# Optimization experiments

Measured on AMD Instinct MI355X. Metric: run time of the kernel, lower is better.

Reference implementation:

```python
import jax, jax.numpy as jnp
import numpy as np

L, B, D, H = 128, 4, 768, 300
NT, NR = 7, 12  # ner tags, relation types
EPS = 1e-5


def _cummax(v):
    # torch: cumsum(softmax(v, -1), -1)
    return jnp.cumsum(jax.nn.softmax(v, axis=-1), axis=-1)


def _layernorm(v, g, b):
    mu = jnp.mean(v, axis=-1, keepdims=True)
    var = jnp.var(v, axis=-1, keepdims=True)
    return (v - mu) * jax.lax.rsqrt(var + EPS) * g + b


def setup_inputs() -> dict:
    key = jax.random.key(0)
    ks = jax.random.split(key, 24)
    s = lambda fan_in: 1.0 / np.sqrt(fan_in)
    u = lambda k, shape, sc: jax.random.uniform(k, shape, jnp.float32, -sc, sc)
    inp = {
        "x": jax.random.normal(ks[0], (L, B, D), jnp.float32),
        "mask": jnp.ones((L, B), jnp.float32),
        # PFN_Unit
        "W_ih": u(ks[1], (5 * H, D), s(D)), "b_ih": u(ks[2], (5 * H,), s(D)),
        "W_hh": u(ks[3], (5 * H, H), s(H)), "b_hh": u(ks[4], (5 * H,), s(H)),
        "W_tr": u(ks[5], (H, 3 * H), s(3 * H)), "b_tr": u(ks[6], (H,), s(3 * H)),
        # NERUnit
        "n_W": u(ks[7], (H, 2 * H), s(2 * H)), "n_b": u(ks[8], (H,), s(2 * H)),
        "ner_hW": u(ks[9], (H, 3 * H), s(3 * H)), "ner_hb": u(ks[10], (H,), s(3 * H)),
        "ner_g": jnp.ones((H,), jnp.float32), "ner_beta": jnp.zeros((H,), jnp.float32),
        "ner_tW": u(ks[11], (NT, H), s(H)), "ner_tb": u(ks[12], (NT,), s(H)),
        # ReUnit
        "r_W": u(ks[13], (H, 2 * H), s(2 * H)), "r_b": u(ks[14], (H,), s(2 * H)),
        "re_hW": u(ks[15], (H, 3 * H), s(3 * H)), "re_hb": u(ks[16], (H,), s(3 * H)),
        "re_g": jnp.ones((H,), jnp.float32), "re_beta": jnp.zeros((H,), jnp.float32),
        "re_tW": u(ks[17], (NR, H), s(H)), "re_tb": u(ks[18], (NR,), s(H)),
    }
    return inp


def _encoder(x, W_ih, b_ih, W_hh, b_hh, W_tr, b_tr):
    pre = jnp.einsum('lbd,gd->lbg', x, W_ih) + b_ih  # precompute input transform [L,B,5H]

    def step(carry, gx):
        h, c_in = carry
        gates = gx + h @ W_hh.T + b_hh
        c, eg_cin, rg_cin, eg_c, rg_c = jnp.split(gates, 5, axis=1)
        eg_cin, rg_cin = 1.0 - _cummax(eg_cin), _cummax(rg_cin)
        eg_c, rg_c = 1.0 - _cummax(eg_c), _cummax(rg_c)
        c = jnp.tanh(c)
        ov_c = rg_c * eg_c
        up_c, dn_c = rg_c - ov_c, eg_c - ov_c
        ov_i = rg_cin * eg_cin
        up_i, dn_i = rg_cin - ov_i, eg_cin - ov_i
        share = ov_i * c_in + ov_c * c
        c_re = up_i * c_in + up_c * c + share
        c_ner = dn_i * c_in + dn_c * c + share
        c_out = jnp.concatenate([c_re, c_ner, share], axis=-1) @ W_tr.T + b_tr
        h_out = jnp.tanh(c_out)
        return (h_out, c_out), (jnp.tanh(c_ner), jnp.tanh(c_re), jnp.tanh(share))

    h0 = jnp.zeros((x.shape[1], W_hh.shape[1]), x.dtype)
    _, (h_ner, h_re, h_share) = jax.lax.scan(step, (h0, h0), pre)
    return h_ner, h_re, h_share  # each [L,B,H]


def _pair_unit(h_task, h_share, mask, gW, gb, hW, hb, ln_g, ln_b, tW, tb, diag):
    length = h_task.shape[0]
    # global feature: tanh(Linear(cat(share, task))), max over time
    h_glob = jnp.tanh(jnp.concatenate([h_share, h_task], axis=-1) @ gW.T + gb)  # [L,B,H]
    g = jnp.max(h_glob, axis=0)  # [B,H]
    # pairwise feature [L,L,B,3H] = cat(start, end, global)
    st = jnp.broadcast_to(h_task[:, None], (length, length) + h_task.shape[1:])
    en = jnp.broadcast_to(h_task[None, :], (length, length) + h_task.shape[1:])
    gb4 = jnp.broadcast_to(g, (length, length) + g.shape)
    feat = jnp.concatenate([st, en, gb4], axis=-1)
    out = _layernorm(feat @ hW.T + hb, ln_g, ln_b)
    out = jax.nn.elu(out)  # eval mode: dropout is identity
    out = jax.nn.sigmoid(out @ tW.T + tb)  # [L,L,B,T]
    # mask
    m = mask[:, None, :] * mask[None, :, :]  # [L,L,B]
    if diag:
        m = m * jnp.triu(jnp.ones((length, length), out.dtype))[:, :, None]
    return out * m[..., None]


def reference(x, mask, W_ih, b_ih, W_hh, b_hh, W_tr, b_tr,
              n_W, n_b, ner_hW, ner_hb, ner_g, ner_beta, ner_tW, ner_tb,
              r_W, r_b, re_hW, re_hb, re_g, re_beta, re_tW, re_tb):
    h_ner, h_re, h_share = _encoder(x, W_ih, b_ih, W_hh, b_hh, W_tr, b_tr)
    ner = _pair_unit(h_ner, h_share, mask, n_W, n_b, ner_hW, ner_hb,
                     ner_g, ner_beta, ner_tW, ner_tb, diag=True)
    re = _pair_unit(h_re, h_share, mask, r_W, r_b, re_hW, re_hb,
                    re_g, re_beta, re_tW, re_tb, diag=False)
    return ner, re
```

## Files before the change

kernel.cpp:

```cpp
#include <hip/hip_runtime.h>

#define LLEN 128
#define BB 4
#define DD 768
#define HH 300
#define G5 1500
#define H3 900
#define NTT 7
#define NRR 12
#define NCHB 10
#define RPB 150
#define OPB 30

#define C_WIH  0
#define C_X    1152000
#define C_WHH2 1545216
#define C_WTR2 1995216
#define F_BIH  2265216
#define F_BTR  2266720
#define F_PRE  2267040
#define F_HG0  (F_PRE)
#define F_HG1  (F_PRE+153600)
#define F_A0   (F_PRE+307200)
#define F_E0   (F_PRE+460800)
#define F_GF0  (F_PRE+616832)
#define F_GF1  (F_PRE+618048)
#define F_HNER (F_PRE+768000)
#define F_HRE  (F_HNER+153600)
#define F_HSH  (F_HRE+153600)
#define F_A1   0
#define F_E1   153600
#define F_AUX  (F_HSH+153600)
#define P_CPUB 192000
#define AUXB   2432
#define AUX_FL 9728
#define WS_NEED_BYTES ((size_t)(F_AUX+11776)*4)

typedef unsigned short u16;
typedef unsigned int u32;
typedef float f4 __attribute__((ext_vector_type(4)));
typedef int i4 __attribute__((ext_vector_type(4)));

__device__ __forceinline__ float bf2f(u16 u) {
  union { u32 i; float f; } v; v.i = ((u32)u) << 16; return v.f;
}
__device__ __forceinline__ u16 f2bf(float f) {
  union { float f; u32 i; } v; v.f = f;
  u32 r = v.i + 0x7fffu + ((v.i >> 16) & 1u);
  return (u16)(r >> 16);
}
__device__ __forceinline__ float ldin(const void* p, int i, bool f32) {
  return f32 ? ((const float*)p)[i] : bf2f(((const u16*)p)[i]);
}
__device__ __forceinline__ bool is32(const void* mk) {
  return ((const u16*)mk)[0] == 0;
}
__device__ __forceinline__ float wsum(float x) {
  #pragma unroll
  for (int d = 1; d < 64; d <<= 1) x += __shfl_xor(x, d);
  return x;
}
__device__ __forceinline__ void astore(float* p, float v) {
  union { float f; int i; } u; u.f = v;
  __hip_atomic_store((int*)p, u.i, __ATOMIC_RELAXED, __HIP_MEMORY_SCOPE_AGENT);
}
__device__ __forceinline__ void gbar(int* flag, int tid, int target) {
  __syncthreads();
  if (tid == 0) {
    __builtin_amdgcn_s_waitcnt(0);
    __hip_atomic_fetch_add(flag, 1, __ATOMIC_RELAXED, __HIP_MEMORY_SCOPE_AGENT);
    int it = 0;
    while (__hip_atomic_load(flag, __ATOMIC_RELAXED, __HIP_MEMORY_SCOPE_AGENT) < target) {
      __builtin_amdgcn_s_sleep(1);
      if (++it > 50000) break;
    }
  }
  __syncthreads();
}
__device__ __forceinline__ f4 ld4x(const f4* p, int mode) {
  f4 v;
  if (mode)
    asm volatile("global_load_dwordx4 %0, %1, off sc0\n\ts_waitcnt vmcnt(0)"
                 : "=v"(v) : "v"(p) : "memory");
  else
    asm volatile("global_load_dwordx4 %0, %1, off sc0 sc1\n\ts_waitcnt vmcnt(0)"
                 : "=v"(v) : "v"(p) : "memory");
  return v;
}
__device__ __forceinline__ float ld1x(const float* p, int mode) {
  float v;
  if (mode)
    asm volatile("global_load_dword %0, %1, off sc0\n\ts_waitcnt vmcnt(0)"
                 : "=v"(v) : "v"(p) : "memory");
  else
    asm volatile("global_load_dword %0, %1, off sc0 sc1\n\ts_waitcnt vmcnt(0)"
                 : "=v"(v) : "v"(p) : "memory");
  return v;
}
__device__ __forceinline__ int ldix(const int* p, int mode) {
  int v;
  if (mode)
    asm volatile("global_load_dword %0, %1, off sc0\n\ts_waitcnt vmcnt(0)"
                 : "=v"(v) : "v"(p) : "memory");
  else
    asm volatile("global_load_dword %0, %1, off sc0 sc1\n\ts_waitcnt vmcnt(0)"
                 : "=v"(v) : "v"(p) : "memory");
  return v;
}
__device__ __forceinline__ void exst(float* p, float v, int mode) {
  if (mode) *p = v; else astore(p, v);
}
__device__ __forceinline__ void ld9(const float* base,
                                    f4& a0, f4& a1, f4& a2, f4& a3, f4& a4,
                                    f4& a5, f4& a6, f4& a7, f4& a8) {
  asm volatile(
    "global_load_dwordx4 %0, %9, off sc0\n\t"
    "global_load_dwordx4 %1, %9, off offset:16 sc0\n\t"
    "global_load_dwordx4 %2, %9, off offset:32 sc0\n\t"
    "global_load_dwordx4 %3, %9, off offset:64 sc0\n\t"
    "global_load_dwordx4 %4, %9, off offset:80 sc0\n\t"
    "global_load_dwordx4 %5, %9, off offset:96 sc0\n\t"
    "global_load_dwordx4 %6, %9, off offset:128 sc0\n\t"
    "global_load_dwordx4 %7, %9, off offset:144 sc0\n\t"
    "global_load_dwordx4 %8, %9, off offset:160 sc0\n\t"
    "s_waitcnt vmcnt(0)"
    : "=&v"(a0), "=&v"(a1), "=&v"(a2), "=&v"(a3), "=&v"(a4),
      "=&v"(a5), "=&v"(a6), "=&v"(a7), "=&v"(a8)
    : "v"(base) : "memory");
}
__device__ __forceinline__ int poll10(const int* slots, int tok, int mode) {
  i4 a, b, c;
  if (mode)
    asm volatile("global_load_dwordx4 %0, %3, off sc0\n\t"
                 "global_load_dwordx4 %1, %4, off sc0\n\t"
                 "global_load_dwordx4 %2, %5, off sc0\n\t"
                 "s_waitcnt vmcnt(0)"
                 : "=&v"(a), "=&v"(b), "=&v"(c)
                 : "v"(slots), "v"(slots + 4), "v"(slots + 8) : "memory");
  else
    asm volatile("global_load_dwordx4 %0, %3, off sc0 sc1\n\t"
                 "global_load_dwordx4 %1, %4, off sc0 sc1\n\t"
                 "global_load_dwordx4 %2, %5, off sc0 sc1\n\t"
                 "s_waitcnt vmcnt(0)"
                 : "=&v"(a), "=&v"(b), "=&v"(c)
                 : "v"(slots), "v"(slots + 4), "v"(slots + 8) : "memory");
  return (a.x >= tok) & (a.y >= tok) & (a.z >= tok) & (a.w >= tok) &
         (b.x >= tok) & (b.y >= tok) & (b.z >= tok) & (b.w >= tok) &
         (c.x >= tok) & (c.y >= tok);
}
__device__ __forceinline__ void sbar(int* slots, int ch, int tok, int tid, int mode) {
  asm volatile("s_waitcnt vmcnt(0)" ::: "memory");
  __syncthreads();
  if (tid == 0) {
    if (mode) slots[ch] = tok;
    else __hip_atomic_store(slots + ch, tok, __ATOMIC_RELAXED, __HIP_MEMORY_SCOPE_AGENT);
  }
  if (tid < 64) {
    int it = 0;
    while (!poll10(slots, tok, mode)) {
      __builtin_amdgcn_s_sleep(1);
      if (++it > 5000) break;
    }
  }
  __syncthreads();
}
__device__ __forceinline__ void sbarA(int* slots, int* abf, int ch, int tok, int tid,
                                      volatile int* s_fail) {
  asm volatile("s_waitcnt vmcnt(0)" ::: "memory");
  __syncthreads();
  if (tid == 0)
    __hip_atomic_store(slots + ch, tok, __ATOMIC_RELAXED, __HIP_MEMORY_SCOPE_AGENT);
  if (tid < 64) {
    int it = 0;
    while (!poll10(slots, tok, 0)) {
      __builtin_amdgcn_s_sleep(1);
      ++it;
      if ((it & 255) == 0 &&
          __hip_atomic_load(abf, __ATOMIC_RELAXED, __HIP_MEMORY_SCOPE_AGENT) != 0) {
        *s_fail = 1; break;
      }
      if (it > 8000) {
        __hip_atomic_store(abf, 1, __ATOMIC_RELAXED, __HIP_MEMORY_SCOPE_AGENT);
        *s_fail = 1; break;
      }
    }
  }
  __syncthreads();
}
__device__ __forceinline__ int claim_bc(int* cl, int nb) {
  unsigned xcd;
  asm volatile("s_getreg_b32 %0, hwreg(HW_REG_XCC_ID)" : "=s"(xcd));
  xcd &= 7u;
  int rank = __hip_atomic_fetch_add(cl + xcd, 1, __ATOMIC_RELAXED, __HIP_MEMORY_SCOPE_AGENT);
  __hip_atomic_fetch_add(cl + 8, 1, __ATOMIC_RELAXED, __HIP_MEMORY_SCOPE_AGENT);
  int it = 0;
  while (__hip_atomic_load(cl + 8, __ATOMIC_RELAXED, __HIP_MEMORY_SCOPE_AGENT) < nb) {
    __builtin_amdgcn_s_sleep(2);
    if (++it > 100000) break;
  }
  int base = 0;
  for (unsigned x = 0; x < xcd; ++x)
    base += __hip_atomic_load(cl + x, __ATOMIC_RELAXED, __HIP_MEMORY_SCOPE_AGENT) / NCHB;
  int cnt = __hip_atomic_load(cl + xcd, __ATOMIC_RELAXED, __HIP_MEMORY_SCOPE_AGENT);
  int slot = base + rank / NCHB;
  return (rank < (cnt / NCHB) * NCHB && slot < BB) ? (slot * 16 + rank % NCHB) : -1;
}

__global__ void k_canon(const void* xo, const void* mk, const void* Wih, const void* bih,
                        const void* Whh, const void* bhh, const void* Wtr, const void* btr,
                        float* ws) {
  bool f32 = is32(mk);
  int piece = blockIdx.y;
  int i = blockIdx.x * 256 + threadIdx.x;
  switch (piece) {
    case 0: if (!f32 && i < 1152000) ws[C_WIH + i] = ldin(Wih, i, f32); break;
    case 1: if (!f32 && i < 393216)  ws[C_X + i]   = ldin(xo, i, f32);  break;
    case 2: if (i < 225000) {
      int k2 = i / G5, out = i - k2 * G5;
      float2 v;
      v.x = ldin(Whh, out * HH + 2 * k2, f32);
      v.y = ldin(Whh, out * HH + 2 * k2 + 1, f32);
      ((float2*)(ws + C_WHH2))[i] = v;
    } break;
    case 3: if (i < 135000) {
      int k2 = i / HH, out = i - k2 * HH;
      float2 v;
      v.x = ldin(Wtr, out * H3 + 2 * k2, f32);
      v.y = ldin(Wtr, out * H3 + 2 * k2 + 1, f32);
      ((float2*)(ws + C_WTR2))[i] = v;
    } break;
    case 4: {
      if (i < 1504) ws[F_BIH + i] = (i < G5) ? ldin(bih, i, f32) + ldin(bhh, i, f32) : 0.f;
      else if (i < 1824) { int j = i - 1504; ws[F_BTR + j] = (j < HH) ? ldin(btr, j, f32) : 0.f; }
    } break;
    case 5: {
      if (i < AUX_FL) ws[F_AUX + i] = 0.f;
      else if (i < 11776) {
        int* ip = (int*)(ws + F_AUX + AUX_FL);
        __hip_atomic_store(ip + (i - AUX_FL), 0, __ATOMIC_RELAXED, __HIP_MEMORY_SCOPE_AGENT);
      }
    } break;
  }
}

__global__ void k_pre2(const void* xo, const void* Wo, const void* mk,
                       const float* cX, const float* cW, const float* biasf, float* pre) {
  bool f32 = is32(mk);
  const float* X = f32 ? (const float*)xo : cX;
  const float* W = f32 ? (const float*)Wo : cW;
  __shared__ __align__(16) float xl[8 * DD];
  int tid = threadIdx.x;
  int lb0 = (blockIdx.x >> 1) * 8;
  int half = blockIdx.x & 1;
  for (int e = tid; e < 8 * DD; e += 256) xl[e] = X[(size_t)lb0 * DD + e];
  __syncthreads();
  for (int j = half * 750 + tid; j < half * 750 + 750; j += 256) {
    const float4* w = (const float4*)(W + (size_t)j * DD);
    float acc[8] = {0.f, 0.f, 0.f, 0.f, 0.f, 0.f, 0.f, 0.f};
    #pragma unroll 2
    for (int k = 0; k < DD / 4; ++k) {
      float4 u = w[k];
      #pragma unroll
      for (int r = 0; r < 8; ++r) {
        const float4 p = *(const float4*)(xl + r * DD + k * 4);
        acc[r] += u.x * p.x + u.y * p.y + u.z * p.z + u.w * p.w;
      }
    }
    float bias = biasf[j];
    #pragma unroll
    for (int r = 0; r < 8; ++r) pre[(size_t)(lb0 + r) * G5 + j] = acc[r] + bias;
  }
}

__global__ void __launch_bounds__(512, 2) k_scanA(const float* pre, const float2* W2h, const float2* W2t,
                                                  const float* btrf, float* hner, float* hre, float* hsh,
                                                  float* aux, float* xw) {
  __shared__ __align__(16) float ga_l[1504];
  __shared__ __align__(16) float vv_l[1204];
  __shared__ __align__(16) float tnh_l[304];
  __shared__ __align__(16) float cat_l[904];
  __shared__ __align__(16) float ci_l[304];
  __shared__ __align__(16) float ps[512];
  __shared__ __align__(16) float h_loc[32];
  __shared__ int s_bc;
  __shared__ int s_fail;
  int tid = threadIdx.x;
  int* ibase = (int*)(aux + AUX_FL);
  if (tid == 0) { s_bc = claim_bc(ibase, (int)gridDim.x); s_fail = 0; }
  __syncthreads();
  int bc = s_bc;
  if (bc < 0) return;
  int b = bc >> 4, ch = bc & 15;
  int* slots = ibase + 32 + b * 64;
  int* abf   = slots + 24;
  int* done  = ibase + 1536;

  if (ch < 2) {
    float* pb0 = xw + (size_t)ch * 96000 + b * 24000;
    for (int i = tid; i < 3000; i += 512) {
      int row = i >> 1, col = 10 + (i & 1);
      pb0[row * 16 + col] = 0.f;
    }
  }

  int o0 = 3 * tid;
  float2 wh2[45];
  if (tid < 500) {
    #pragma unroll
    for (int j = 0; j < 3; ++j)
      #pragma unroll
      for (int kk = 0; kk < 15; ++kk)
        wh2[j * 15 + kk] = W2h[(size_t)(ch * 15 + kk) * G5 + (o0 + j)];
  }
  int o2 = tid % OPB, jj = tid / OPB;
  float2 wt[29];
  int k2b = jj * 29;
  int k2e = (k2b + 29 < 450) ? (k2b + 29) : 450;
  int nk2 = k2e - k2b;
  if (tid < 480) {
    const float2* wp = W2t + (size_t)k2b * HH + (ch * OPB + o2);
    #pragma unroll
    for (int q = 0; q < 29; ++q) if (q < nk2) wt[q] = wp[(size_t)q * HH];
  }
  float pv0 = 0.f, pv1 = 0.f, pv2 = 0.f;
  if (tid < 500) {
    const float* pr = pre + (size_t)b * G5 + o0;
    pv0 = pr[0]; pv1 = pr[1]; pv2 = pr[2];
  }
  __syncthreads();

  for (int t = 0; t < LLEN; ++t) {
    int buf = t & 1;
    float* pb = xw + (size_t)buf * 96000 + b * 24000;
    if (t > 0) {
      if (tid < 500) {
        float2 h2[15];
        #pragma unroll
        for (int kk = 0; kk < 15; ++kk) h2[kk] = *(const float2*)(h_loc + 2 * kk);
        #pragma unroll
        for (int j = 0; j < 3; ++j) {
          float acc = 0.f;
          #pragma unroll
          for (int kk = 0; kk < 15; ++kk)
            acc += wh2[j * 15 + kk].x * h2[kk].x + wh2[j * 15 + kk].y * h2[kk].y;
          pb[(size_t)(o0 + j) * 16 + ch] = acc;
        }
      }
      sbarA(slots, abf, ch, t, tid, &s_fail);
      if (s_fail) return;
      if (tid < 500) {
        f4 a0, a1, a2, a3, a4, a5, a6, a7, a8;
        ld9(pb + (size_t)o0 * 16, a0, a1, a2, a3, a4, a5, a6, a7, a8);
        ga_l[o0]     = pv0 + (((a0.x + a0.y) + (a0.z + a0.w)) +
                              ((a1.x + a1.y) + (a1.z + a1.w)) +
                              ((a2.x + a2.y) + (a2.z + a2.w)));
        ga_l[o0 + 1] = pv1 + (((a3.x + a3.y) + (a3.z + a3.w)) +
                              ((a4.x + a4.y) + (a4.z + a4.w)) +
                              ((a5.x + a5.y) + (a5.z + a5.w)));
        ga_l[o0 + 2] = pv2 + (((a6.x + a6.y) + (a6.z + a6.w)) +
                              ((a7.x + a7.y) + (a7.z + a7.w)) +
                              ((a8.x + a8.y) + (a8.z + a8.w)));
      }
      if (tid < 75) {
        const float* cp = xw + P_CPUB + (size_t)(((t - 1) & 1) * 4 + b) * 304;
        f4 v = ld4x((const f4*)cp + tid, 1);
        *(f4*)(ci_l + 4 * tid) = v;
      }
    } else {
      if (tid < 500) { ga_l[o0] = pv0; ga_l[o0 + 1] = pv1; ga_l[o0 + 2] = pv2; }
    }
    __syncthreads();
    if (tid < HH) tnh_l[tid] = tanhf(ga_l[tid]);
    {
      int w = tid >> 6, ln = tid & 63;
      if (w >= 4) {
        int c = w - 3;
        const float* g = ga_l + c * 300;
        int e0 = ln * 5;
        float ex0 = 0.f, ex1 = 0.f, ex2 = 0.f, ex3 = 0.f, ex4 = 0.f;
        if (ln < 60) {
          ex0 = __expf(g[e0]); ex1 = __expf(g[e0 + 1]); ex2 = __expf(g[e0 + 2]);
          ex3 = __expf(g[e0 + 3]); ex4 = __expf(g[e0 + 4]);
        }
        float p = ((ex0 + ex1) + (ex2 + ex3)) + ex4;
        float inc = p;
        #pragma unroll
        for (int d = 1; d < 64; d <<= 1) { float o = __shfl_up(inc, d); if (ln >= d) inc += o; }
        float S = __shfl(inc, 59);
        float invS = 1.f / S;
        float run = inc - p;
        if (ln < 60) {
          float* vv = vv_l + (c - 1) * 300 + e0;
          run += ex0; vv[0] = run * invS;
          run += ex1; vv[1] = run * invS;
          run += ex2; vv[2] = run * invS;
          run += ex3; vv[3] = run * invS;
          run += ex4; vv[4] = run * invS;
        }
      }
    }
    if (t + 1 < LLEN && tid < 500) {
      const float* pr = pre + ((size_t)(t + 1) * BB + b) * G5 + o0;
      pv0 = pr[0]; pv1 = pr[1]; pv2 = pr[2];
    }
    __syncthreads();
    if (tid < HH) {
      float c = tnh_l[tid];
      float v0 = vv_l[tid], v1 = vv_l[300 + tid], v2 = vv_l[600 + tid], v3 = vv_l[900 + tid];
      float eg_cin = 1.f - v0, rg_cin = v1, eg_c = 1.f - v2, rg_c = v3;
      float ci = (t > 0) ? ci_l[tid] : 0.f;
      float ov_c = rg_c * eg_c;
      float up_c = rg_c - ov_c, dn_c = eg_c - ov_c;
      float ov_i = rg_cin * eg_cin;
      float up_i = rg_cin - ov_i, dn_i = eg_cin - ov_i;
      float share = ov_i * ci + ov_c * c;
      float c_re  = up_i * ci + up_c * c + share;
      float c_ner = dn_i * ci + dn_c * c + share;
      cat_l[tid] = c_re; cat_l[HH + tid] = c_ner; cat_l[2 * HH + tid] = share;
      int sb = ch * OPB;
      if (tid >= sb && tid < sb + OPB) {
        size_t ob = ((size_t)t * BB + b) * HH + tid;
        hner[ob] = tanhf(c_ner); hre[ob] = tanhf(c_re); hsh[ob] = tanhf(share);
      }
    }
    __syncthreads();
    if (tid < 480) {
      float acc = 0.f;
      #pragma unroll
      for (int q = 0; q < 29; ++q)
        if (q < nk2) acc += wt[q].x * cat_l[2 * (k2b + q)] + wt[q].y * cat_l[2 * (k2b + q) + 1];
      ps[tid] = acc;
    }
    __syncthreads();
    if (tid < OPB) {
      float co = btrf[ch * OPB + tid];
      #pragma unroll
      for (int q = 0; q < 16; ++q) co += ps[q * OPB + tid];
      h_loc[tid] = tanhf(co);
      float* cp = xw + P_CPUB + (size_t)(buf * 4 + b) * 304;
      cp[ch * OPB + tid] = co;
    }
    __syncthreads();
  }
  if (tid == 0 && s_fail == 0)
    __hip_atomic_fetch_add(done + b, 1, __ATOMIC_RELAXED, __HIP_MEMORY_SCOPE_AGENT);
}

__global__ void __launch_bounds__(512, 2) k_scanB(const float* pre, const float2* W2h, const float2* W2t,
                                                  const float* btrf, float* hner, float* hre, float* hsh,
                                                  float* aux) {
  __shared__ __align__(16) float h_l[304];
  __shared__ __align__(16) float ci_l[304];
  __shared__ __align__(16) float ga_l[1504];
  __shared__ __align__(16) float cat_l[904];
  __shared__ __align__(16) float ps[512];
  __shared__ __align__(16) float sums_l[8];
  __shared__ float exv[160];
  __shared__ int s_bc, s_mode, s_skip;
  int tid = threadIdx.x;
  int* ibase = (int*)(aux + AUX_FL);
  int* cl2 = ibase + 640;
  if (tid == 0) s_bc = claim_bc(cl2, (int)gridDim.x);
  __syncthreads();
  int bc = s_bc;
  if (bc < 0) return;
  int b = bc >> 4, ch = bc & 15;
  int* done = ibase + 1536;
  if (tid == 0)
    s_skip = (__hip_atomic_load(done + b, __ATOMIC_RELAXED, __HIP_MEMORY_SCOPE_AGENT) == NCHB);
  __syncthreads();
  if (s_skip) return;
  int s = ch >> 1;
  int r0 = ch * RPB;
  float* gb   = aux + b * AUXB;
  float* cb   = gb + 1504;
  float* hb   = gb + 1808;
  float* sums = gb + 2112;
  int* slotsA = ibase + 672 + b * 64;
  int* slotsB = slotsA + 16;
  int* atf    = slotsA + 32;

  {
    float* tst = gb + 2240;
    int* seflag = (int*)(gb + 2272);
    if (ch == 0 && tid == 0) tst[0] = 1.0f;
    gbar(atf + 0, tid, NCHB);
    if (tid == 0) { float w1 = ld1x(tst, 1); (void)w1; }
    gbar(atf + 1, tid, NCHB);
    if (ch == 0 && tid == 0) { tst[0] = 2.0f; __builtin_amdgcn_s_waitcnt(0); }
    if (ch == 1 && tid == 0)
      __hip_atomic_fetch_add(seflag, 1, __ATOMIC_RELAXED, __HIP_MEMORY_SCOPE_WORKGROUP);
    gbar(atf + 2, tid, NCHB);
    if (tid == 0) {
      float w2 = ld1x(tst, 1);
      int fv = ldix(seflag, 1);
      if (w2 != 2.0f || fv != 1)
        __hip_atomic_fetch_or(atf + 4, 1, __ATOMIC_RELAXED, __HIP_MEMORY_SCOPE_AGENT);
    }
    gbar(atf + 3, tid, NCHB);
    if (tid == 0)
      s_mode = (__hip_atomic_load(atf + 4, __ATOMIC_RELAXED, __HIP_MEMORY_SCOPE_AGENT) == 0) ? 1 : 0;
    __syncthreads();
  }
  int mode = s_mode;

  int j = tid / RPB, r = tid - j * RPB;
  int o2 = tid % OPB, jj = tid / OPB;
  int kb = j * 100;

  float2 wh[50];
  if (tid < 450) {
    const float2* wp = W2h + (size_t)(j * 50) * G5 + (r0 + r);
    #pragma unroll
    for (int kk = 0; kk < 50; ++kk) wh[kk] = wp[(size_t)kk * G5];
  }
  float2 wt[29];
  int k2b = jj * 29;
  int k2e = (k2b + 29 < 450) ? (k2b + 29) : 450;
  int nk2 = k2e - k2b;
  if (tid < 480) {
    const float2* wp = W2t + (size_t)k2b * HH + (ch * OPB + o2);
    #pragma unroll
    for (int q = 0; q < 29; ++q) if (q < nk2) wt[q] = wp[(size_t)q * HH];
  }
  float pv = 0.f;
  if (tid < RPB) pv = pre[(size_t)b * G5 + r0 + tid];
  __syncthreads();

  for (int t = 0; t < LLEN; ++t) {
    if (t > 0) {
      if (tid < 75)       { f4 v = ld4x((const f4*)hb + tid, mode); *(f4*)(h_l + 4 * tid) = v; }
      else if (tid < 150) { int q = tid - 75; f4 v = ld4x((const f4*)cb + q, mode); *(f4*)(ci_l + 4 * q) = v; }
      __syncthreads();
    }
    if (tid < 450) {
      float acc = (j == 0) ? pv : 0.f;
      if (t > 0) {
        #pragma unroll
        for (int kk = 0; kk < 50; ++kk)
          acc += wh[kk].x * h_l[kb + 2 * kk] + wh[kk].y * h_l[kb + 2 * kk + 1];
      }
      ps[tid] = acc;
    }
    __syncthreads();
    if (tid < RPB) {
      float g = ps[tid] + ps[RPB + tid] + ps[2 * RPB + tid];
      if (s == 0) exst(gb + r0 + tid, tanhf(g), mode);
      else exv[tid] = __expf(g);
    }
    if (s > 0) {
      __syncthreads();
      if (tid < 30) {
        int base2 = tid * 5;
        float e0 = exv[base2], e1 = exv[base2 + 1], e2 = exv[base2 + 2],
              e3 = exv[base2 + 3], e4 = exv[base2 + 4];
        float p = ((e0 + e1) + (e2 + e3)) + e4;
        float inc = p;
        #pragma unroll
        for (int d = 1; d < 32; d <<= 1) { float o = __shfl_up(inc, d); if (tid >= d) inc += o; }
        float tot = __shfl(inc, 29);
        float run = inc - p;
        run += e0; exst(gb + r0 + base2,     run, mode);
        run += e1; exst(gb + r0 + base2 + 1, run, mode);
        run += e2; exst(gb + r0 + base2 + 2, run, mode);
        run += e3; exst(gb + r0 + base2 + 3, run, mode);
        run += e4; exst(gb + r0 + base2 + 4, run, mode);
        if (tid == 0) exst(sums + (ch - 2), tot, mode);
      }
    }
    sbar(slotsA, ch, t + 1, tid, mode);
    if (tid < 375)      { f4 v = ld4x((const f4*)gb + tid, mode); *(f4*)(ga_l + 4 * tid) = v; }
    else if (tid < 377) { int q = tid - 375; f4 v = ld4x((const f4*)sums + q, mode); *(f4*)(sums_l + 4 * q) = v; }
    float pvn = 0.f;
    if (t + 1 < LLEN && tid < RPB) pvn = pre[((size_t)(t + 1) * BB + b) * G5 + r0 + tid];
    __syncthreads();
    if (tid < HH) {
      float c = ga_l[tid];
      float v[4];
      #pragma unroll
      for (int s1 = 0; s1 < 4; ++s1) {
        float raw = ga_l[(s1 + 1) * HH + tid];
        float off = (tid >= RPB) ? sums_l[2 * s1] : 0.f;
        float S = sums_l[2 * s1] + sums_l[2 * s1 + 1];
        v[s1] = (raw + off) / S;
      }
      float eg_cin = 1.f - v[0], rg_cin = v[1], eg_c = 1.f - v[2], rg_c = v[3];
      float ci = (t > 0) ? ci_l[tid] : 0.f;
      float ov_c = rg_c * eg_c;
      float up_c = rg_c - ov_c, dn_c = eg_c - ov_c;
      float ov_i = rg_cin * eg_cin;
      float up_i = rg_cin - ov_i, dn_i = eg_cin - ov_i;
      float share = ov_i * ci + ov_c * c;
      float c_re  = up_i * ci + up_c * c + share;
      float c_ner = dn_i * ci + dn_c * c + share;
      cat_l[tid] = c_re; cat_l[HH + tid] = c_ner; cat_l[2 * HH + tid] = share;
      int sb = ch * OPB;
      if (tid >= sb && tid < sb + OPB) {
        size_t ob = ((size_t)t * BB + b) * HH + tid;
        hner[ob] = tanhf(c_ner); hre[ob] = tanhf(c_re); hsh[ob] = tanhf(share);
      }
    }
    __syncthreads();
    if (tid < 480) {
      float acc = 0.f;
      #pragma unroll
      for (int q = 0; q < 29; ++q)
        if (q < nk2) acc += wt[q].x * cat_l[2 * (k2b + q)] + wt[q].y * cat_l[2 * (k2b + q) + 1];
      ps[tid] = acc;
    }
    __syncthreads();
    if (tid < OPB) {
      float co = btrf[ch * OPB + tid];
      #pragma unroll
      for (int q = 0; q < 16; ++q) co += ps[q * OPB + tid];
      exst(cb + ch * OPB + tid, co, mode);
      exst(hb + ch * OPB + tid, tanhf(co), mode);
    }
    if (t + 1 < LLEN) sbar(slotsB, ch, t + 1, tid, mode);
    pv = pvn;
  }
}

__global__ void k_glob3(const float* hsh, const float* hner, const float* hre,
                        const void* nW, const void* nb, const void* rW, const void* rb,
                        const void* mk, float* hg0, float* hg1) {
  bool f32 = is32(mk);
  int task = blockIdx.x >> 7;
  int lb0 = (blockIdx.x & 127) * 4;
  const float* tsk = task ? hre : hner;
  const void* gWo = task ? rW : nW;
  const void* gbo = task ? rb : nb;
  float* hg = task ? hg1 : hg0;
  __shared__ __align__(16) float catl[2400];
  int tid = threadIdx.x;
  for (int e = tid; e < 2400; e += 320) {
    int rr = e / 600, c = e - rr * 600;
    catl[e] = (c < HH) ? hsh[(size_t)(lb0 + rr) * HH + c] : tsk[(size_t)(lb0 + rr) * HH + (c - HH)];
  }
  __syncthreads();
  if (tid < HH) {
    float bias = ldin(gbo, tid, f32);
    float acc[4] = {bias, bias, bias, bias};
    if (f32) {
      const float4* row = (const float4*)((const float*)gWo + (size_t)tid * 600);
      #pragma unroll 2
      for (int k = 0; k < 150; ++k) {
        float4 u = row[k];
        #pragma unroll
        for (int rr = 0; rr < 4; ++rr) {
          const float4 cv = *(const float4*)(catl + rr * 600 + 4 * k);
          acc[rr] += u.x * cv.x + u.y * cv.y + u.z * cv.z + u.w * cv.w;
        }
      }
    } else {
      for (int k = 0; k < 600; ++k) {
        float w = ldin(gWo, tid * 600 + k, f32);
        #pragma unroll
        for (int rr = 0; rr < 4; ++rr) acc[rr] += w * catl[rr * 600 + k];
      }
    }
    #pragma unroll
    for (int rr = 0; rr < 4; ++rr) hg[(size_t)(lb0 + rr) * HH + tid] = tanhf(acc[rr]);
  }
}

__global__ void k_feat2(const float* hner, const float* hre,
                        const void* nhW, const void* nhb, const void* rhW, const void* rhb,
                        const void* mk, float* A0, float* E0, float* A1, float* E1) {
  bool f32 = is32(mk);
  int task = blockIdx.x >> 7;
  int lb0 = (blockIdx.x & 127) * 4;
  const float* tsk = task ? hre : hner;
  const void* hWo = task ? rhW : nhW;
  const void* hbo = task ? rhb : nhb;
  float* A = task ? A1 : A0;
  float* E = task ? E1 : E0;
  __shared__ __align__(16) float tl[1200];
  int tid = threadIdx.x;
  for (int e = tid; e < 1200; e += 320) {
    int rr = e / 300, c = e - rr * 300;
    tl[e] = tsk[(size_t)(lb0 + rr) * HH + c];
  }
  __syncthreads();
  if (tid < HH) {
    float bias = ldin(hbo, tid, f32);
    float a[4] = {bias, bias, bias, bias};
    float ev[4] = {0.f, 0.f, 0.f, 0.f};
    if (f32) {
      const float4* r1 = (const float4*)((const float*)hWo + (size_t)tid * H3);
      const float4* r2 = (const float4*)((const float*)hWo + (size_t)tid * H3 + HH);
      #pragma unroll 2
      for (int k = 0; k < 75; ++k) {
        float4 u = r1[k], w2 = r2[k];
        #pragma unroll
        for (int rr = 0; rr < 4; ++rr) {
          const float4 tv = *(const float4*)(tl + rr * 300 + 4 * k);
          a[rr]  += u.x * tv.x + u.y * tv.y + u.z * tv.z + u.w * tv.w;
          ev[rr] += w2.x * tv.x + w2.y * tv.y + w2.z * tv.z + w2.w * tv.w;
        }
      }
    } else {
      for (int k = 0; k < HH; ++k) {
        float w1 = ldin(hWo, tid * H3 + k, f32);
        float w2 = ldin(hWo, tid * H3 + HH + k, f32);
        #pragma unroll
        for (int rr = 0; rr < 4; ++rr) {
          a[rr] += w1 * tl[rr * 300 + k];
          ev[rr] += w2 * tl[rr * 300 + k];
        }
      }
    }
    #pragma unroll
    for (int rr = 0; rr < 4; ++rr) {
      A[(size_t)(lb0 + rr) * HH + tid] = a[rr];
      E[(size_t)(lb0 + rr) * HH + tid] = ev[rr];
    }
  }
}

__global__ void k_gmf(const float* hg0, const float* hg1, const void* nhW, const void* rhW,
                      const void* mk, float* Gf0, float* Gf1) {
  bool f32 = is32(mk);
  int task = blockIdx.x >> 2, b = blockIdx.x & 3;
  const float* hg = task ? hg1 : hg0;
  const void* hWo = task ? rhW : nhW;
  float* Gf = task ? Gf1 : Gf0;
  __shared__ __align__(16) float gl[304];
  int tid = threadIdx.x;
  if (tid < HH) {
    float m = -1e30f;
    for (int l = 0; l < LLEN; ++l) m = fmaxf(m, hg[((size_t)l * BB + b) * HH + tid]);
    gl[tid] = m;
  }
  __syncthreads();
  if (tid < HH) {
    float acc = 0.f;
    if (f32) {
      const float4* row = (const float4*)((const float*)hWo + (size_t)tid * H3 + 600);
      #pragma unroll 5
      for (int k = 0; k < 75; ++k) {
        float4 u = row[k];
        const float4 gv = *(const float4*)(gl + 4 * k);
        acc += u.x * gv.x + u.y * gv.y + u.z * gv.z + u.w * gv.w;
      }
    } else {
      for (int k = 0; k < HH; ++k) acc += gl[k] * ldin(hWo, tid * H3 + 600 + k, f32);
    }
    Gf[b * HH + tid] = acc;
  }
}

__global__ void __launch_bounds__(256) k_pair6(const float* A0, const float* E0, const float* Gf0,
                                               const void* lg0, const void* lb0_, const void* tW0, const void* tb0,
                                               const float* A1, const float* E1, const float* Gf1,
                                               const void* lg1, const void* lb1_, const void* tW1, const void* tb1,
                                               const void* mk, void* outv) {
  __shared__ float lg_l[304], lb_l[304], tb_l[16];
  __shared__ float tw_l[3616];
  bool f32 = is32(mk);
  int tau = blockIdx.x >> 12;
  int bid = blockIdx.x & 4095;
  const float* A  = tau ? A1 : A0;
  const float* E  = tau ? E1 : E0;
  const float* Gf = tau ? Gf1 : Gf0;
  const void* lgo = tau ? lg1 : lg0;
  const void* lbo = tau ? lb1_ : lb0_;
  const void* tWo = tau ? tW1 : tW0;
  const void* tbo = tau ? tb1 : tb0;
  int T = tau ? NRR : NTT;
  int diag = tau ? 0 : 1;
  int Toff = tau ? 458752 : 0;
  int tid = threadIdx.x;
  for (int i2 = tid; i2 < HH; i2 += 256) { lg_l[i2] = ldin(lgo, i2, f32); lb_l[i2] = ldin(lbo, i2, f32); }
  for (int i2 = tid; i2 < T * HH; i2 += 256) tw_l[i2] = ldin(tWo, i2, f32);
  if (tid < T) tb_l[tid] = ldin(tbo, tid, f32);
  __syncthreads();
  int i = bid >> 5;
  int j0 = (bid & 31) << 2;
  int b = tid >> 6, ln = tid & 63;
  const float* ar = A  + (size_t)(i * BB + b) * HH;
  const float* gr = Gf + (size_t)b * HH;
  bool ok4 = ln < 44;
  float a0 = ar[ln]       + gr[ln];
  float a1 = ar[64 + ln]  + gr[64 + ln];
  float a2 = ar[128 + ln] + gr[128 + ln];
  float a3 = ar[192 + ln] + gr[192 + ln];
  float a4 = ok4 ? (ar[256 + ln] + gr[256 + ln]) : 0.f;
  float mi = ldin(mk, i * BB + b, f32);
  for (int dj = 0; dj < 4; ++dj) {
    int jx = j0 + dj;
    const float* er = E + (size_t)(jx * BB + b) * HH;
    float u0 = a0 + er[ln];
    float u1 = a1 + er[64 + ln];
    float u2 = a2 + er[128 + ln];
    float u3 = a3 + er[192 + ln];
    float u4 = ok4 ? (a4 + er[256 + ln]) : 0.f;
    float s1 = ((u0 + u1) + (u2 + u3)) + u4;
    float s2 = ((u0 * u0 + u1 * u1) + (u2 * u2 + u3 * u3)) + u4 * u4;
    #pragma unroll
    for (int d = 1; d < 64; d <<= 1) { s1 += __shfl_xor(s1, d); s2 += __shfl_xor(s2, d); }
    float mean = s1 * (1.f / 300.f);
    float var = s2 * (1.f / 300.f) - mean * mean;
    float rstd = rsqrtf(var + 1e-5f);
    {
      float y;
      y = (u0 - mean) * rstd * lg_l[ln]       + lb_l[ln];       u0 = (y > 0.f) ? y : __expf(y) - 1.f;
      y = (u1 - mean) * rstd * lg_l[64 + ln]  + lb_l[64 + ln];  u1 = (y > 0.f) ? y : __expf(y) - 1.f;
      y = (u2 - mean) * rstd * lg_l[128 + ln] + lb_l[128 + ln]; u2 = (y > 0.f) ? y : __expf(y) - 1.f;
      y = (u3 - mean) * rstd * lg_l[192 + ln] + lb_l[192 + ln]; u3 = (y > 0.f) ? y : __expf(y) - 1.f;
      if (ok4) {
        y = (u4 - mean) * rstd * lg_l[256 + ln] + lb_l[256 + ln];
        u4 = (y > 0.f) ? y : __expf(y) - 1.f;
      }
    }
    float m = mi * ldin(mk, jx * BB + b, f32);
    if (diag && jx < i) m = 0.f;
    size_t obase = (size_t)Toff + ((size_t)(i * LLEN + jx) * BB + b) * T;
    float mine = 0.f;
    for (int t = 0; t < T; ++t) {
      const float* twr = tw_l + t * HH;
      float s = u0 * twr[ln] + u1 * twr[64 + ln] + u2 * twr[128 + ln] + u3 * twr[192 + ln];
      if (ok4) s += u4 * twr[256 + ln];
      s = wsum(s);
      s += tb_l[t];
      float o = m / (1.f + __expf(-s));
      mine = (ln == t) ? o : mine;
    }
    if (ln < T) {
      if (f32) ((float*)outv)[obase + ln] = mine;
      else ((u16*)outv)[obase + ln] = f2bf(mine);
    }
  }
}

__global__ void k_sent(const void* mk, const void* xo, void* outv, int hostcode) {
  __shared__ int bad;
  if (threadIdx.x == 0) bad = 0;
  __syncthreads();
  bool f32 = is32(mk);
  for (int i = threadIdx.x; i < 4096; i += 256) {
    float v = ldin(xo, i, f32);
    if (!(v == v) || fabsf(v) > 1e6f) bad = 1;
  }
  __syncthreads();
  if (threadIdx.x == 0) {
    float code = (float)hostcode;
    if (bad) code = fmaxf(code, 88.f);
    if (code > 0.f) {
      if (f32) ((float*)outv)[0] = code;
      else ((u16*)outv)[0] = f2bf(code);
    }
  }
}

extern "C" void kernel_launch(void* const* d_in, const int* in_sizes, int n_in,
                              void* d_out, int out_size, void* d_ws, size_t ws_size,
                              hipStream_t stream) {
  const void* x    = d_in[0];
  const void* mask = d_in[1];
  const void* Wih  = d_in[2];
  const void* bih  = d_in[3];
  const void* Whh  = d_in[4];
  const void* bhh  = d_in[5];
  const void* Wtr  = d_in[6];
  const void* btr  = d_in[7];
  const void* nW   = d_in[8];
  const void* nb   = d_in[9];
  const void* nhW  = d_in[10];
  const void* nhb  = d_in[11];
  const void* ng   = d_in[12];
  const void* nbe  = d_in[13];
  const void* ntW  = d_in[14];
  const void* ntb  = d_in[15];
  const void* rW   = d_in[16];
  const void* rb   = d_in[17];
  const void* rhW  = d_in[18];
  const void* rhb  = d_in[19];
  const void* rg   = d_in[20];
  const void* rbe  = d_in[21];
  const void* rtW  = d_in[22];
  const void* rtb  = d_in[23];
  float* ws = (float*)d_ws;

  static const int exp_sz[24] = {393216, 512, 1152000, 1500, 450000, 1500, 270000, 300,
                                 180000, 300, 270000, 300, 300, 300, 2100, 7,
                                 180000, 300, 270000, 300, 300, 300, 3600, 12};
  int hostcode = 0;
  if (n_in != 24) hostcode = 890;
  else {
    for (int ii = 0; ii < 24; ++ii)
      if (in_sizes[ii] != exp_sz[ii]) { hostcode = 900 + ii; break; }
  }
  if (hostcode == 0 && out_size != 1245184) hostcode = 880;
  if (hostcode == 0 && ws_size < WS_NEED_BYTES) hostcode = 1099;

  dim3 gc(4500, 6);
  k_canon<<<gc, 256, 0, stream>>>(x, mask, Wih, bih, Whh, bhh, Wtr, btr, ws);
  k_pre2<<<128, 256, 0, stream>>>(x, Wih, mask, ws + C_X, ws + C_WIH, ws + F_BIH, ws + F_PRE);
  k_scanA<<<256, 512, 0, stream>>>(ws + F_PRE, (const float2*)(ws + C_WHH2), (const float2*)(ws + C_WTR2),
                                   ws + F_BTR, ws + F_HNER, ws + F_HRE, ws + F_HSH, ws + F_AUX, ws);
  k_scanB<<<256, 512, 0, stream>>>(ws + F_PRE, (const float2*)(ws + C_WHH2), (const float2*)(ws + C_WTR2),
                                   ws + F_BTR, ws + F_HNER, ws + F_HRE, ws + F_HSH, ws + F_AUX);
  k_glob3<<<256, 320, 0, stream>>>(ws + F_HSH, ws + F_HNER, ws + F_HRE,
                                   nW, nb, rW, rb, mask, ws + F_HG0, ws + F_HG1);
  k_feat2<<<256, 320, 0, stream>>>(ws + F_HNER, ws + F_HRE, nhW, nhb, rhW, rhb, mask,
                                   ws + F_A0, ws + F_E0, ws + F_A1, ws + F_E1);
  k_gmf<<<8, 320, 0, stream>>>(ws + F_HG0, ws + F_HG1, nhW, rhW, mask, ws + F_GF0, ws + F_GF1);
  k_pair6<<<8192, 256, 0, stream>>>(ws + F_A0, ws + F_E0, ws + F_GF0, ng, nbe, ntW, ntb,
                                    ws + F_A1, ws + F_E1, ws + F_GF1, rg, rbe, rtW, rtb,
                                    mask, d_out);
  k_sent<<<1, 256, 0, stream>>>(mask, x, d_out, hostcode);
}
```

Before: 1.438 ms.

## Merge post-scan GEMVs, skip lower-triangle NER tiles, shrink grids

Merges the global-context and feature projection kernels into one launch that selects its role by block index, cutting one kernel launch. The pair kernel now handles 8 columns per block instead of 4, and NER blocks lying entirely below the diagonal just write zeros and exit without loading weights or computing. The canon kernel becomes grid-stride with 512 blocks instead of 4500, and the scan kernels launch 128 blocks instead of 256. Halving the scan grid may change how the slot-claiming logic distributes blocks across XCDs, which could affect correctness or parallelism of the recurrence.

```diff
diff --git a/kernel.cpp b/kernel.cpp
--- a/kernel.cpp
+++ b/kernel.cpp
@@ -211,31 +211,32 @@
                         float* ws) {
   bool f32 = is32(mk);
   int piece = blockIdx.y;
-  int i = blockIdx.x * 256 + threadIdx.x;
+  int i0 = blockIdx.x * 256 + threadIdx.x;
+  int stride = gridDim.x * 256;
   switch (piece) {
-    case 0: if (!f32 && i < 1152000) ws[C_WIH + i] = ldin(Wih, i, f32); break;
-    case 1: if (!f32 && i < 393216)  ws[C_X + i]   = ldin(xo, i, f32);  break;
-    case 2: if (i < 225000) {
+    case 0: if (!f32) for (int i = i0; i < 1152000; i += stride) ws[C_WIH + i] = ldin(Wih, i, f32); break;
+    case 1: if (!f32) for (int i = i0; i < 393216; i += stride) ws[C_X + i] = ldin(xo, i, f32); break;
+    case 2: for (int i = i0; i < 225000; i += stride) {
       int k2 = i / G5, out = i - k2 * G5;
       float2 v;
       v.x = ldin(Whh, out * HH + 2 * k2, f32);
       v.y = ldin(Whh, out * HH + 2 * k2 + 1, f32);
       ((float2*)(ws + C_WHH2))[i] = v;
     } break;
-    case 3: if (i < 135000) {
+    case 3: for (int i = i0; i < 135000; i += stride) {
       int k2 = i / HH, out = i - k2 * HH;
       float2 v;
       v.x = ldin(Wtr, out * H3 + 2 * k2, f32);
       v.y = ldin(Wtr, out * H3 + 2 * k2 + 1, f32);
       ((float2*)(ws + C_WTR2))[i] = v;
     } break;
-    case 4: {
+    case 4: for (int i = i0; i < 1824; i += stride) {
       if (i < 1504) ws[F_BIH + i] = (i < G5) ? ldin(bih, i, f32) + ldin(bhh, i, f32) : 0.f;
-      else if (i < 1824) { int j = i - 1504; ws[F_BTR + j] = (j < HH) ? ldin(btr, j, f32) : 0.f; }
+      else { int j = i - 1504; ws[F_BTR + j] = (j < HH) ? ldin(btr, j, f32) : 0.f; }
     } break;
-    case 5: {
+    case 5: for (int i = i0; i < 11776; i += stride) {
       if (i < AUX_FL) ws[F_AUX + i] = 0.f;
-      else if (i < 11776) {
+      else {
         int* ip = (int*)(ws + F_AUX + AUX_FL);
         __hip_atomic_store(ip + (i - AUX_FL), 0, __ATOMIC_RELAXED, __HIP_MEMORY_SCOPE_AGENT);
       }
@@ -621,99 +622,96 @@
   }
 }
 
-__global__ void k_glob3(const float* hsh, const float* hner, const float* hre,
-                        const void* nW, const void* nb, const void* rW, const void* rb,
-                        const void* mk, float* hg0, float* hg1) {
+__global__ void k_post(const float* hsh, const float* hner, const float* hre,
+                       const void* nW, const void* nb, const void* rW, const void* rb,
+                       const void* nhW, const void* nhb, const void* rhW, const void* rhb,
+                       const void* mk, float* hg0, float* hg1,
+                       float* A0, float* E0, float* A1, float* E1) {
   bool f32 = is32(mk);
-  int task = blockIdx.x >> 7;
-  int lb0 = (blockIdx.x & 127) * 4;
-  const float* tsk = task ? hre : hner;
-  const void* gWo = task ? rW : nW;
-  const void* gbo = task ? rb : nb;
-  float* hg = task ? hg1 : hg0;
-  __shared__ __align__(16) float catl[2400];
+  int role = blockIdx.x >> 8;
+  int sub  = blockIdx.x & 255;
+  int task = sub >> 7;
+  int lb0 = (sub & 127) * 4;
+  __shared__ __align__(16) float buf[2400];
   int tid = threadIdx.x;
-  for (int e = tid; e < 2400; e += 320) {
-    int rr = e / 600, c = e - rr * 600;
-    catl[e] = (c < HH) ? hsh[(size_t)(lb0 + rr) * HH + c] : tsk[(size_t)(lb0 + rr) * HH + (c - HH)];
-  }
-  __syncthreads();
-  if (tid < HH) {
-    float bias = ldin(gbo, tid, f32);
-    float acc[4] = {bias, bias, bias, bias};
-    if (f32) {
-      const float4* row = (const float4*)((const float*)gWo + (size_t)tid * 600);
-      #pragma unroll 2
-      for (int k = 0; k < 150; ++k) {
-        float4 u = row[k];
-        #pragma unroll
-        for (int rr = 0; rr < 4; ++rr) {
-          const float4 cv = *(const float4*)(catl + rr * 600 + 4 * k);
-          acc[rr] += u.x * cv.x + u.y * cv.y + u.z * cv.z + u.w * cv.w;
+  if (role == 0) {
+    const float* tsk = task ? hre : hner;
+    const void* gWo = task ? rW : nW;
+    const void* gbo = task ? rb : nb;
+    float* hg = task ? hg1 : hg0;
+    for (int e = tid; e < 2400; e += 320) {
+      int rr = e / 600, c = e - rr * 600;
+      buf[e] = (c < HH) ? hsh[(size_t)(lb0 + rr) * HH + c] : tsk[(size_t)(lb0 + rr) * HH + (c - HH)];
+    }
+    __syncthreads();
+    if (tid < HH) {
+      float bias = ldin(gbo, tid, f32);
+      float acc[4] = {bias, bias, bias, bias};
+      if (f32) {
+        const float4* row = (const float4*)((const float*)gWo + (size_t)tid * 600);
+        #pragma unroll 2
+        for (int k = 0; k < 150; ++k) {
+          float4 u = row[k];
+          #pragma unroll
+          for (int rr = 0; rr < 4; ++rr) {
+            const float4 cv = *(const float4*)(buf + rr * 600 + 4 * k);
+            acc[rr] += u.x * cv.x + u.y * cv.y + u.z * cv.z + u.w * cv.w;
+          }
         }
-      }
-    } else {
-      for (int k = 0; k < 600; ++k) {
-        float w = ldin(gWo, tid * 600 + k, f32);
-        #pragma unroll
-        for (int rr = 0; rr < 4; ++rr) acc[rr] += w * catl[rr * 600 + k];
-      }
-    }
-    #pragma unroll
-    for (int rr = 0; rr < 4; ++rr) hg[(size_t)(lb0 + rr) * HH + tid] = tanhf(acc[rr]);
-  }
-}
-
-__global__ void k_feat2(const float* hner, const float* hre,
-                        const void* nhW, const void* nhb, const void* rhW, const void* rhb,
-                        const void* mk, float* A0, float* E0, float* A1, float* E1) {
-  bool f32 = is32(mk);
-  int task = blockIdx.x >> 7;
-  int lb0 = (blockIdx.x & 127) * 4;
-  const float* tsk = task ? hre : hner;
-  const void* hWo = task ? rhW : nhW;
-  const void* hbo = task ? rhb : nhb;
-  float* A = task ? A1 : A0;
-  float* E = task ? E1 : E0;
-  __shared__ __align__(16) float tl[1200];
-  int tid = threadIdx.x;
-  for (int e = tid; e < 1200; e += 320) {
-    int rr = e / 300, c = e - rr * 300;
-    tl[e] = tsk[(size_t)(lb0 + rr) * HH + c];
-  }
-  __syncthreads();
-  if (tid < HH) {
-    float bias = ldin(hbo, tid, f32);
-    float a[4] = {bias, bias, bias, bias};
-    float ev[4] = {0.f, 0.f, 0.f, 0.f};
-    if (f32) {
-      const float4* r1 = (const float4*)((const float*)hWo + (size_t)tid * H3);
-      const float4* r2 = (const float4*)((const float*)hWo + (size_t)tid * H3 + HH);
-      #pragma unroll 2
-      for (int k = 0; k < 75; ++k) {
-        float4 u = r1[k], w2 = r2[k];
-        #pragma unroll
-        for (int rr = 0; rr < 4; ++rr) {
-          const float4 tv = *(const float4*)(tl + rr * 300 + 4 * k);
-          a[rr]  += u.x * tv.x + u.y * tv.y + u.z * tv.z + u.w * tv.w;
-          ev[rr] += w2.x * tv.x + w2.y * tv.y + w2.z * tv.z + w2.w * tv.w;
+      } else {
+        for (int k = 0; k < 600; ++k) {
+          float w = ldin(gWo, tid * 600 + k, f32);
+          #pragma unroll
+          for (int rr = 0; rr < 4; ++rr) acc[rr] += w * buf[rr * 600 + k];
         }
       }
-    } else {
-      for (int k = 0; k < HH; ++k) {
-        float w1 = ldin(hWo, tid * H3 + k, f32);
-        float w2 = ldin(hWo, tid * H3 + HH + k, f32);
-        #pragma unroll
-        for (int rr = 0; rr < 4; ++rr) {
-          a[rr] += w1 * tl[rr * 300 + k];
-          ev[rr] += w2 * tl[rr * 300 + k];
+      #pragma unroll
+      for (int rr = 0; rr < 4; ++rr) hg[(size_t)(lb0 + rr) * HH + tid] = tanhf(acc[rr]);
+    }
+  } else {
+    const float* tsk = task ? hre : hner;
+    const void* hWo = task ? rhW : nhW;
+    const void* hbo = task ? rhb : nhb;
+    float* A = task ? A1 : A0;
+    float* E = task ? E1 : E0;
+    for (int e = tid; e < 1200; e += 320) {
+      int rr = e / 300, c = e - rr * 300;
+      buf[e] = tsk[(size_t)(lb0 + rr) * HH + c];
+    }
+    __syncthreads();
+    if (tid < HH) {
+      float bias = ldin(hbo, tid, f32);
+      float a[4] = {bias, bias, bias, bias};
+      float ev[4] = {0.f, 0.f, 0.f, 0.f};
+      if (f32) {
+        const float4* r1 = (const float4*)((const float*)hWo + (size_t)tid * H3);
+        const float4* r2 = (const float4*)((const float*)hWo + (size_t)tid * H3 + HH);
+        #pragma unroll 2
+        for (int k = 0; k < 75; ++k) {
+          float4 u = r1[k], w2 = r2[k];
+          #pragma unroll
+          for (int rr = 0; rr < 4; ++rr) {
+            const float4 tv = *(const float4*)(buf + rr * 300 + 4 * k);
+            a[rr]  += u.x * tv.x + u.y * tv.y + u.z * tv.z + u.w * tv.w;
+            ev[rr] += w2.x * tv.x + w2.y * tv.y + w2.z * tv.z + w2.w * tv.w;
+          }
         }
-      }
-    }
-    #pragma unroll
-    for (int rr = 0; rr < 4; ++rr) {
-      A[(size_t)(lb0 + rr) * HH + tid] = a[rr];
-      E[(size_t)(lb0 + rr) * HH + tid] = ev[rr];
+      } else {
+        for (int k = 0; k < HH; ++k) {
+          float w1 = ldin(hWo, tid * H3 + k, f32);
+          float w2 = ldin(hWo, tid * H3 + HH + k, f32);
+          #pragma unroll
+          for (int rr = 0; rr < 4; ++rr) {
+            a[rr] += w1 * buf[rr * 300 + k];
+            ev[rr] += w2 * buf[rr * 300 + k];
+          }
+        }
+      }
+      #pragma unroll
+      for (int rr = 0; rr < 4; ++rr) {
+        A[(size_t)(lb0 + rr) * HH + tid] = a[rr];
+        E[(size_t)(lb0 + rr) * HH + tid] = ev[rr];
+      }
     }
   }
 }
@@ -750,7 +748,7 @@
   }
 }
 
-__global__ void __launch_bounds__(256) k_pair6(const float* A0, const float* E0, const float* Gf0,
+__global__ void __launch_bounds__(256) k_pair7(const float* A0, const float* E0, const float* Gf0,
                                                const void* lg0, const void* lb0_, const void* tW0, const void* tb0,
                                                const float* A1, const float* E1, const float* Gf1,
                                                const void* lg1, const void* lb1_, const void* tW1, const void* tb1,
@@ -758,8 +756,26 @@
   __shared__ float lg_l[304], lb_l[304], tb_l[16];
   __shared__ float tw_l[3616];
   bool f32 = is32(mk);
-  int tau = blockIdx.x >> 12;
-  int bid = blockIdx.x & 4095;
+  int tau = blockIdx.x >> 11;
+  int bid = blockIdx.x & 2047;
+  int i = bid >> 4;
+  int j0 = (bid & 15) << 3;
+  int T = tau ? NRR : NTT;
+  int diag = tau ? 0 : 1;
+  int Toff = tau ? 458752 : 0;
+  int tid = threadIdx.x;
+  int b = tid >> 6, ln = tid & 63;
+  if (diag && j0 + 7 < i) {
+    if (ln < T) {
+      #pragma unroll
+      for (int dj = 0; dj < 8; ++dj) {
+        size_t obase = (size_t)Toff + ((size_t)(i * LLEN + j0 + dj) * BB + b) * T;
+        if (f32) ((float*)outv)[obase + ln] = 0.f;
+        else ((u16*)outv)[obase + ln] = 0;
+      }
+    }
+    return;
+  }
   const float* A  = tau ? A1 : A0;
   const float* E  = tau ? E1 : E0;
   const float* Gf = tau ? Gf1 : Gf0;
@@ -767,17 +783,10 @@
   const void* lbo = tau ? lb1_ : lb0_;
   const void* tWo = tau ? tW1 : tW0;
   const void* tbo = tau ? tb1 : tb0;
-  int T = tau ? NRR : NTT;
-  int diag = tau ? 0 : 1;
-  int Toff = tau ? 458752 : 0;
-  int tid = threadIdx.x;
   for (int i2 = tid; i2 < HH; i2 += 256) { lg_l[i2] = ldin(lgo, i2, f32); lb_l[i2] = ldin(lbo, i2, f32); }
   for (int i2 = tid; i2 < T * HH; i2 += 256) tw_l[i2] = ldin(tWo, i2, f32);
   if (tid < T) tb_l[tid] = ldin(tbo, tid, f32);
   __syncthreads();
-  int i = bid >> 5;
-  int j0 = (bid & 31) << 2;
-  int b = tid >> 6, ln = tid & 63;
   const float* ar = A  + (size_t)(i * BB + b) * HH;
   const float* gr = Gf + (size_t)b * HH;
   bool ok4 = ln < 44;
@@ -787,7 +796,7 @@
   float a3 = ar[192 + ln] + gr[192 + ln];
   float a4 = ok4 ? (ar[256 + ln] + gr[256 + ln]) : 0.f;
   float mi = ldin(mk, i * BB + b, f32);
-  for (int dj = 0; dj < 4; ++dj) {
+  for (int dj = 0; dj < 8; ++dj) {
     int jx = j0 + dj;
     const float* er = E + (size_t)(jx * BB + b) * HH;
     float u0 = a0 + er[ln];
@@ -894,19 +903,18 @@
   if (hostcode == 0 && out_size != 1245184) hostcode = 880;
   if (hostcode == 0 && ws_size < WS_NEED_BYTES) hostcode = 1099;
 
-  dim3 gc(4500, 6);
+  dim3 gc(512, 6);
   k_canon<<<gc, 256, 0, stream>>>(x, mask, Wih, bih, Whh, bhh, Wtr, btr, ws);
   k_pre2<<<128, 256, 0, stream>>>(x, Wih, mask, ws + C_X, ws + C_WIH, ws + F_BIH, ws + F_PRE);
-  k_scanA<<<256, 512, 0, stream>>>(ws + F_PRE, (const float2*)(ws + C_WHH2), (const float2*)(ws + C_WTR2),
+  k_scanA<<<128, 512, 0, stream>>>(ws + F_PRE, (const float2*)(ws + C_WHH2), (const float2*)(ws + C_WTR2),
                                    ws + F_BTR, ws + F_HNER, ws + F_HRE, ws + F_HSH, ws + F_AUX, ws);
-  k_scanB<<<256, 512, 0, stream>>>(ws + F_PRE, (const float2*)(ws + C_WHH2), (const float2*)(ws + C_WTR2),
+  k_scanB<<<128, 512, 0, stream>>>(ws + F_PRE, (const float2*)(ws + C_WHH2), (const float2*)(ws + C_WTR2),
                                    ws + F_BTR, ws + F_HNER, ws + F_HRE, ws + F_HSH, ws + F_AUX);
-  k_glob3<<<256, 320, 0, stream>>>(ws + F_HSH, ws + F_HNER, ws + F_HRE,
-                                   nW, nb, rW, rb, mask, ws + F_HG0, ws + F_HG1);
-  k_feat2<<<256, 320, 0, stream>>>(ws + F_HNER, ws + F_HRE, nhW, nhb, rhW, rhb, mask,
-                                   ws + F_A0, ws + F_E0, ws + F_A1, ws + F_E1);
+  k_post<<<512, 320, 0, stream>>>(ws + F_HSH, ws + F_HNER, ws + F_HRE,
+                                  nW, nb, rW, rb, nhW, nhb, rhW, rhb, mask,
+                                  ws + F_HG0, ws + F_HG1, ws + F_A0, ws + F_E0, ws + F_A1, ws + F_E1);
   k_gmf<<<8, 320, 0, stream>>>(ws + F_HG0, ws + F_HG1, nhW, rhW, mask, ws + F_GF0, ws + F_GF1);
-  k_pair6<<<8192, 256, 0, stream>>>(ws + F_A0, ws + F_E0, ws + F_GF0, ng, nbe, ntW, ntb,
+  k_pair7<<<4096, 256, 0, stream>>>(ws + F_A0, ws + F_E0, ws + F_GF0, ng, nbe, ntW, ntb,
                                     ws + F_A1, ws + F_E1, ws + F_GF1, rg, rbe, rtW, rtb,
                                     mask, d_out);
   k_sent<<<1, 256, 0, stream>>>(mask, x, d_out, hostcode);
```

Result: faster. 1.367 ms (-4.9%).
